# Optimization experiments

Hardware: AMD Instinct MI355X
Metric: run time of the kernel (lower is better)

Reference implementation:

```python
import jax, jax.numpy as jnp
import numpy as np

RATE = 0.001
N_ITERS = 100
EPS = 1e-7


def setup_inputs() -> dict:
    key = jax.random.key(0)
    k1, k2 = jax.random.split(key)
    # hazy image in (0.05, 0.9) so 1 - img/airlight stays positive
    img = jax.random.uniform(k1, (1024, 1024, 3), dtype=jnp.float32) * 0.85 + 0.05
    # airlight near 1 (bright atmospheric light)
    airlight = jax.random.uniform(k2, (3,), dtype=jnp.float32) * 0.05 + 0.95
    return {"img": img, "airlight": airlight, "patch_size": 7}


def _grad1d(x):
    # np.gradient along last axis: one-sided at edges, central in interior. x: [3, N]
    left = x[:, 1:2] - x[:, 0:1]
    mid = (x[:, 2:] - x[:, :-2]) * 0.5
    right = x[:, -1:] - x[:, -2:-1]
    return jnp.concatenate([left, mid, right], axis=1)


def reference(img, airlight, patch_size):
    p = int(patch_size)
    h, w = img.shape[0], img.shape[1]
    hp, wp = h - p, w - p
    N = hp * wp
    A = airlight  # [3]

    # tlb[i,j] = max_c (1 - patch_center/airlight); patch center offset = p//2
    center = img[p // 2:p // 2 + hp, p // 2:p // 2 + wp, :]  # [hp,wp,3]
    tlb = jnp.max(1.0 - center / A, axis=-1)  # [hp,wp]
    img_c = img[:hp, :wp, :]  # cropped image [hp,wp,3]

    def dehaze(t):  # Eq: L = (I - A)/t + A
        return (img_c - A) / t[..., None] + A  # [hp,wp,3]

    def compute_sig(l_img):
        # faithful to original: np.reshape(l_img,[3,-1]) is a raw reshape (not transpose)
        l3 = jnp.reshape(l_img, (3, N))
        g = _grad1d(l3)                      # [3, N]
        y = jnp.reshape(g, (N, 3))           # raw reshape [-1,3] as in original
        l2 = jnp.sqrt(jnp.sum(y * y, axis=1))
        return jax.nn.sigmoid(-48.0 * (l2 - 0.1)).reshape(hp, wp)

    def loss_fn(wgt, sig):
        lg = jnp.log(wgt)
        # conv2d with [-1,0,1] kernel, zero padding (0,1): dx = lg[:,j+1]-lg[:,j-1]
        lpx = jnp.pad(lg, ((0, 0), (1, 1)))
        dx = lpx[:, 2:] - lpx[:, :-2]
        # conv2d with [1,0,-1]^T kernel, zero padding (1,0): dy = lg[i-1,:]-lg[i+1,:]
        lpy = jnp.pad(lg, ((1, 1), (0, 0)))
        dy = lpy[:-2, :] - lpy[2:, :]
        return jnp.sum((dx * dx + dy * dy) * sig)

    def body(carry, _):
        t_prev, sig = carry
        w0 = jnp.where(t_prev <= 0, EPS, t_prev)      # clamp as in minimization()
        g = jax.grad(loss_fn)(w0, sig)
        t_curr = w0 - RATE * g                         # one SGD step
        sig_new = compute_sig(dehaze(t_curr))
        return (t_curr, sig_new), None

    sig0 = compute_sig(dehaze(tlb))
    (t_final, _), _ = jax.lax.scan(body, (tlb, sig0), None, length=N_ITERS)
    return dehaze(t_final)  # [hp, wp, 3]
```

## Files before the change

### kernel.cpp

```cpp
#include <hip/hip_runtime.h>

#define HP    1017
#define WP    1017
#define NPIX  (HP*WP)
#define N3    (NPIX/3)
#define W_IMG 1024
#define EPSV  1e-7f

#define K_ITERS 4
#define RY   48
#define CW   48
#define HALO 8
#define IY   64
#define IC   64
#define NBX  22
#define NBY  22
#define TBT  512
#define NSLOT 8
#define WQMAX 1551431

typedef _Float16 half_t;

__device__ __forceinline__ float fast_rcp(float x) { return __builtin_amdgcn_rcpf(x); }

__global__ void init_kernel(const float* __restrict__ img, const float* __restrict__ A,
                            half_t* __restrict__ img_c, float* __restrict__ t0) {
    int b = blockIdx.x * blockDim.x + threadIdx.x;
    int a = blockIdx.y;
    if (b >= WP) return;
    int m = a * WP + b;
    float A0 = A[0], A1 = A[1], A2 = A[2];
    const float* src = img + ((size_t)a * W_IMG + b) * 3;
    img_c[3*m+0] = (half_t)src[0];
    img_c[3*m+1] = (half_t)src[1];
    img_c[3*m+2] = (half_t)src[2];
    const float* cen = img + ((size_t)(a+3) * W_IMG + (b+3)) * 3;
    float t = 1.0f - cen[0] / A0;
    t = fmaxf(t, 1.0f - cen[1] / A1);
    t = fmaxf(t, 1.0f - cen[2] / A2);
    t0[m] = t;
}

__global__ __launch_bounds__(TBT, 6) void tb_kernel(
    const float* __restrict__ tin, float* __restrict__ tout,
    const half_t* __restrict__ img_c, const float* __restrict__ A)
{
    __shared__ float  lgl[2][IY][IC];
    __shared__ half_t sgl[IY][IC];
    __shared__ half_t rll[IY][IC];

    const int tid   = threadIdx.x;
    const int i0    = tid >> 6;
    const int j     = tid & 63;
    const int rbase = blockIdx.y * RY - HALO;
    const int cbase = blockIdx.x * CW - HALO;
    const int col   = cbase + j;
    const float A0 = A[0], A1 = A[1], A2 = A[2];

    const int da = (col < 0) ? -1 : ((col >= WP) ? 1 : 0);
    const int b  = col - da * WP;
    const bool bW  = (b >= 1), bW2 = (b >= 2);
    const bool bE  = (b <= WP-2), bE2 = (b <= WP-3);
    const int m00 = (rbase + i0) * WP + col;

    const unsigned* imgw = (const unsigned*)img_c;
    unsigned pk01[NSLOT], pk12[NSLOT], pk3[NSLOT/2];
    float w0r[NSLOT];
    float rB[NSLOT];

    {
        int m = m00;
        #pragma unroll
        for (int s = 0; s < NSLOT; ++s, m += 8*WP) {
            int i = i0 + 8*s;
            float v = 1.0f;
            if ((unsigned)m < (unsigned)NPIX) v = tin[m];
            float rv = fast_rcp(v);
            w0r[s] = (v <= 0.0f) ? EPSV : v;
            rB[s]  = rv;
            rll[i][j]    = (half_t)rv;
            lgl[0][i][j] = __logf(v <= 0.0f ? EPSV : v);
            int hb = 3*m - 1;
            int wq, off0;
            if (m <= 0) { wq = 0; off0 = 0; }
            else        { wq = hb >> 1; off0 = 1 + (hb & 1); if (wq > WQMAX) wq = WQMAX; }
            unsigned w0 = imgw[wq], w1 = imgw[wq+1], w2 = imgw[wq+2];
            unsigned pa, pb; unsigned f3h;
            if (off0 == 0)      { pa = (w0 & 0xffffu) | (w0 << 16); pb = (w0 >> 16) | (w1 << 16); f3h = w2 & 0xffffu; }
            else if (off0 == 1) { pa = w0;                          pb = w1;                      f3h = w2 & 0xffffu; }
            else                { pa = (w0 >> 16) | (w1 << 16);     pb = (w1 >> 16) | (w2 << 16); f3h = w2 >> 16; }
            if (m >= NPIX - 1) f3h = (pb >> 16);
            pk01[s] = pa; pk12[s] = pb;
            if (s & 1) pk3[s >> 1] |= (f3h << 16);
            else       pk3[s >> 1]  = f3h;
        }
    }
    __syncthreads();

    #pragma unroll
    for (int lvl = 0; lvl < K_ITERS; ++lvl) {
        float (* __restrict__ lgc)[IC] = lgl[lvl & 1];
        float (* __restrict__ lgn)[IC] = lgl[(lvl & 1) ^ 1];
        const int ms = 2*lvl + 1;
        const bool jokB = (j >= ms && j < IC - ms);
        {
            int m = m00;
            #pragma unroll
            for (int s = 0; s < NSLOT; ++s, m += 8*WP) {
                int i = i0 + 8*s;
                float sv = 0.0f;
                if (jokB && i >= ms && i < IY - ms && (unsigned)m < (unsigned)NPIX) {
                    float r0 = rB[s];
                    float rm = (m > 0)        ? (float)rll[i][j-1] : r0;
                    float rp = (m < NPIX - 1) ? (float)rll[i][j+1] : r0;
                    union { unsigned u; half_t h[2]; } ua, ub, uc;
                    ua.u = pk01[s]; ub.u = pk12[s]; uc.u = pk3[s >> 1];
                    float fm1 = (float)ua.h[0];
                    float f0  = (float)ua.h[1];
                    float f1  = (float)ub.h[0];
                    float f2  = (float)ub.h[1];
                    float f3  = (float)uc.h[s & 1];
                    float dm1 = (fm1 - A2) * rm + A2;
                    float d0  = (f0  - A0) * r0 + A0;
                    float d1  = (f1  - A1) * r0 + A1;
                    float d2  = (f2  - A2) * r0 + A2;
                    float d3  = (f3  - A0) * rp + A0;
                    float y0 = 0.5f * (d1 - dm1);
                    float y1 = 0.5f * (d2 - d0);
                    float y2 = 0.5f * (d3 - d1);
                    if (m == 0      ) y0 = d1 - d0;
                    if (m == N3     ) y0 = d1 - d0;
                    if (m == 2*N3   ) y0 = d1 - d0;
                    if (m == N3 - 1 ) y2 = d2 - d1;
                    if (m == 2*N3-1 ) y2 = d2 - d1;
                    if (m == NPIX-1 ) y2 = d2 - d1;
                    float l2 = sqrtf(y0*y0 + y1*y1 + y2*y2);
                    sv = fast_rcp(1.0f + __expf(48.0f * (l2 - 0.1f)));
                }
                sgl[i][j] = (half_t)sv;
            }
        }
        __syncthreads();
        const int mt = 2*lvl + 2;
        const bool jokC = (j >= mt && j < IC - mt);
        {
            int m = m00;
            #pragma unroll
            for (int s = 0; s < NSLOT; ++s, m += 8*WP) {
                int i = i0 + 8*s;
                if (jokC && i >= mt && i < IY - mt && (unsigned)m < (unsigned)NPIX) {
                    int a = rbase + i + da;
                    float lgC = lgc[i][j];
                    float acc = 0.0f;
                    if (bW)
                        acc += (lgC - (bW2 ? lgc[i][j-2] : 0.0f)) * (float)sgl[i][j-1];
                    if (bE)
                        acc -= ((bE2 ? lgc[i][j+2] : 0.0f) - lgC) * (float)sgl[i][j+1];
                    if (a <= HP-2)
                        acc += (lgC - ((a <= HP-3) ? lgc[i+2][j] : 0.0f)) * (float)sgl[i+1][j];
                    if (a >= 1)
                        acc -= (((a >= 2) ? lgc[i-2][j] : 0.0f) - lgC) * (float)sgl[i-1][j];
                    float rr = rB[s];
                    float rw = (rr <= 0.0f) ? 1e7f : rr;
                    float v = w0r[s] - 0.001f * 2.0f * acc * rw;
                    if (lvl == K_ITERS - 1) {
                        if (col < WP) tout[m] = v;
                    } else {
                        float rv = fast_rcp(v);
                        w0r[s] = (v <= 0.0f) ? EPSV : v;
                        rB[s]  = rv;
                        lgn[i][j] = __logf(v <= 0.0f ? EPSV : v);
                        rll[i][j] = (half_t)rv;
                    }
                }
            }
        }
        __syncthreads();
    }
}

__global__ void out_kernel(const float* __restrict__ t, const half_t* __restrict__ img_c,
                           const float* __restrict__ A, float* __restrict__ out) {
    int m = blockIdx.x * blockDim.x + threadIdx.x;
    if (m >= NPIX) return;
    float tv = t[m];
    float A0 = A[0], A1 = A[1], A2 = A[2];
    float r = 1.0f / tv;
    out[3*m+0] = ((float)img_c[3*m+0] - A0) * r + A0;
    out[3*m+1] = ((float)img_c[3*m+1] - A1) * r + A1;
    out[3*m+2] = ((float)img_c[3*m+2] - A2) * r + A2;
}

extern "C" void kernel_launch(void* const* d_in, const int* in_sizes, int n_in,
                              void* d_out, int out_size, void* d_ws, size_t ws_size,
                              hipStream_t stream) {
    const float* img = (const float*)d_in[0];
    const float* A   = (const float*)d_in[1];
    float*  ws    = (float*)d_ws;
    float*  t_a   = ws;
    float*  t_b   = t_a + NPIX;
    half_t* img_c = (half_t*)(t_b + NPIX);

    dim3 blk2(256, 1, 1);
    dim3 grd2((WP + 255) / 256, HP, 1);
    int blk1 = 256;
    int grd1 = (NPIX + blk1 - 1) / blk1;

    hipLaunchKernelGGL(init_kernel, grd2, blk2, 0, stream, img, A, img_c, t_a);

    float* tsrc = t_a;
    float* tdst = t_b;
    for (int d = 0; d < 25; ++d) {
        hipLaunchKernelGGL(tb_kernel, dim3(NBX, NBY), dim3(TBT), 0, stream,
                           tsrc, tdst, img_c, A);
        float* tmp = tsrc; tsrc = tdst; tdst = tmp;
    }
    hipLaunchKernelGGL(out_kernel, dim3(grd1), dim3(blk1), 0, stream,
                       tsrc, img_c, A, (float*)d_out);
}
```

Baseline: 841.1 us.

## Fuse dehaze output into last temporal-block pass and shuffle neighbor reciprocals

Removes the separate output kernel by having the final tb_kernel launch write the dehazed image directly, using the packed image halves already held in registers. Replaces the half-precision shared-memory reciprocal array with wavefront shuffles (neighbors j±1 live in adjacent lanes of the 64-wide row), dropping one barrier and LDS traffic. It also guards the edge-case gradient checks behind a column test. The shuffled values are now full fp32 rather than fp16, which slightly changes numerics, and the final output uses an exact division.

```diff
diff --git a/kernel.cpp b/kernel.cpp
--- a/kernel.cpp
+++ b/kernel.cpp
@@ -43,11 +43,11 @@
 
 __global__ __launch_bounds__(TBT, 6) void tb_kernel(
     const float* __restrict__ tin, float* __restrict__ tout,
-    const half_t* __restrict__ img_c, const float* __restrict__ A)
+    const half_t* __restrict__ img_c, const float* __restrict__ A,
+    float* __restrict__ out, int last)
 {
     __shared__ float  lgl[2][IY][IC];
     __shared__ half_t sgl[IY][IC];
-    __shared__ half_t rll[IY][IC];
 
     const int tid   = threadIdx.x;
     const int i0    = tid >> 6;
@@ -75,10 +75,8 @@
             int i = i0 + 8*s;
             float v = 1.0f;
             if ((unsigned)m < (unsigned)NPIX) v = tin[m];
-            float rv = fast_rcp(v);
             w0r[s] = (v <= 0.0f) ? EPSV : v;
-            rB[s]  = rv;
-            rll[i][j]    = (half_t)rv;
+            rB[s]  = fast_rcp(v);
             lgl[0][i][j] = __logf(v <= 0.0f ? EPSV : v);
             int hb = 3*m - 1;
             int wq, off0;
@@ -95,7 +93,6 @@
             else       pk3[s >> 1]  = f3h;
         }
     }
-    __syncthreads();
 
     #pragma unroll
     for (int lvl = 0; lvl < K_ITERS; ++lvl) {
@@ -108,11 +105,13 @@
             #pragma unroll
             for (int s = 0; s < NSLOT; ++s, m += 8*WP) {
                 int i = i0 + 8*s;
+                float r0  = rB[s];
+                float rup = __shfl_up(r0, 1);
+                float rdn = __shfl_down(r0, 1);
                 float sv = 0.0f;
                 if (jokB && i >= ms && i < IY - ms && (unsigned)m < (unsigned)NPIX) {
-                    float r0 = rB[s];
-                    float rm = (m > 0)        ? (float)rll[i][j-1] : r0;
-                    float rp = (m < NPIX - 1) ? (float)rll[i][j+1] : r0;
+                    float rm = (m > 0)        ? rup : r0;
+                    float rp = (m < NPIX - 1) ? rdn : r0;
                     union { unsigned u; half_t h[2]; } ua, ub, uc;
                     ua.u = pk01[s]; ub.u = pk12[s]; uc.u = pk3[s >> 1];
                     float fm1 = (float)ua.h[0];
@@ -128,12 +127,11 @@
                     float y0 = 0.5f * (d1 - dm1);
                     float y1 = 0.5f * (d2 - d0);
                     float y2 = 0.5f * (d3 - d1);
-                    if (m == 0      ) y0 = d1 - d0;
-                    if (m == N3     ) y0 = d1 - d0;
-                    if (m == 2*N3   ) y0 = d1 - d0;
-                    if (m == N3 - 1 ) y2 = d2 - d1;
-                    if (m == 2*N3-1 ) y2 = d2 - d1;
-                    if (m == NPIX-1 ) y2 = d2 - d1;
+                    if (b == 0) {
+                        if (m == 0 || m == N3 || m == 2*N3) y0 = d1 - d0;
+                    } else if (b == WP-1) {
+                        if (m == N3-1 || m == 2*N3-1 || m == NPIX-1) y2 = d2 - d1;
+                    }
                     float l2 = sqrtf(y0*y0 + y1*y1 + y2*y2);
                     sv = fast_rcp(1.0f + __expf(48.0f * (l2 - 0.1f)));
                 }
@@ -164,31 +162,29 @@
                     float rw = (rr <= 0.0f) ? 1e7f : rr;
                     float v = w0r[s] - 0.001f * 2.0f * acc * rw;
                     if (lvl == K_ITERS - 1) {
-                        if (col < WP) tout[m] = v;
+                        if (col < WP) {
+                            if (last) {
+                                union { unsigned u; half_t h[2]; } ua, ub;
+                                ua.u = pk01[s]; ub.u = pk12[s];
+                                float rr2 = 1.0f / v;
+                                int o = 3*m;
+                                out[o+0] = ((float)ua.h[1] - A0) * rr2 + A0;
+                                out[o+1] = ((float)ub.h[0] - A1) * rr2 + A1;
+                                out[o+2] = ((float)ub.h[1] - A2) * rr2 + A2;
+                            } else {
+                                tout[m] = v;
+                            }
+                        }
                     } else {
-                        float rv = fast_rcp(v);
                         w0r[s] = (v <= 0.0f) ? EPSV : v;
-                        rB[s]  = rv;
+                        rB[s]  = fast_rcp(v);
                         lgn[i][j] = __logf(v <= 0.0f ? EPSV : v);
-                        rll[i][j] = (half_t)rv;
                     }
                 }
             }
         }
         __syncthreads();
     }
-}
-
-__global__ void out_kernel(const float* __restrict__ t, const half_t* __restrict__ img_c,
-                           const float* __restrict__ A, float* __restrict__ out) {
-    int m = blockIdx.x * blockDim.x + threadIdx.x;
-    if (m >= NPIX) return;
-    float tv = t[m];
-    float A0 = A[0], A1 = A[1], A2 = A[2];
-    float r = 1.0f / tv;
-    out[3*m+0] = ((float)img_c[3*m+0] - A0) * r + A0;
-    out[3*m+1] = ((float)img_c[3*m+1] - A1) * r + A1;
-    out[3*m+2] = ((float)img_c[3*m+2] - A2) * r + A2;
 }
 
 extern "C" void kernel_launch(void* const* d_in, const int* in_sizes, int n_in,
@@ -203,8 +199,6 @@
 
     dim3 blk2(256, 1, 1);
     dim3 grd2((WP + 255) / 256, HP, 1);
-    int blk1 = 256;
-    int grd1 = (NPIX + blk1 - 1) / blk1;
 
     hipLaunchKernelGGL(init_kernel, grd2, blk2, 0, stream, img, A, img_c, t_a);
 
@@ -212,9 +206,7 @@
     float* tdst = t_b;
     for (int d = 0; d < 25; ++d) {
         hipLaunchKernelGGL(tb_kernel, dim3(NBX, NBY), dim3(TBT), 0, stream,
-                           tsrc, tdst, img_c, A);
+                           tsrc, tdst, img_c, A, (float*)d_out, (d == 24) ? 1 : 0);
         float* tmp = tsrc; tsrc = tdst; tdst = tmp;
     }
-    hipLaunchKernelGGL(out_kernel, dim3(grd1), dim3(blk1), 0, stream,
-                       tsrc, img_c, A, (float*)d_out);
 }
```

Result: slower. 927.0 us (+10.2%).
